# Optimization experiments

Measured on AMD Instinct MI355X. Metric: run time of the kernel, lower is better.

## Reference

```python
import math
import jax, jax.numpy as jnp
import numpy as np

# --- model constants (from TECAN.__init__ defaults) ---
N = 180
DT = 0.02
SIGMA = 40.0
V_PREF = 22.0
RHO_DEG = 0.5
K = 0.0005
WR = 0.94
W_VS = 0.2
TAU = 1.0
RHO_W = 1.0 / RHO_DEG  # 2.0

B, T = 256, 1024


def _circ(a, b):
    return (a - b + 180.0) % 360.0 - 180.0


def setup_inputs() -> dict:
    key = jax.random.key(0)
    k_vel, k_bv, k_ro = jax.random.split(key, 3)

    xs = jnp.linspace(-180.0, 180.0 - 1.0 / RHO_DEG, N)
    coeff = WR / (math.sqrt(2 * math.pi) * SIGMA) * RHO_W
    gauss = lambda d: jnp.exp(-d ** 2 / (2 * SIGMA ** 2))
    W_r = coeff * gauss(_circ(xs[:, None], xs[None, :]))
    W_plus = coeff * gauss(_circ(xs[:, None], xs[None, :] + V_PREF))
    W_minus = coeff * gauss(_circ(xs[:, None], xs[None, :] - V_PREF))

    U_peak = WR * (1 + math.sqrt(1 - 0.896 ** 2 / WR ** 2)) / (4 * math.sqrt(math.pi) * K * SIGMA)
    u_s0 = U_peak * jnp.exp(-xs ** 2 / (4 * SIGMA ** 2))
    h_init = jnp.concatenate([u_s0, jnp.zeros_like(u_s0), jnp.zeros_like(u_s0)])  # [3N]

    vel = jax.random.normal(k_vel, (B, T, 1), dtype=jnp.float32)
    B_v = jax.random.normal(k_bv, (1,), dtype=jnp.float32) / 10.0
    # torch Linear(N,1,bias=False) init: U(-1/sqrt(N), 1/sqrt(N))
    readout_W = jax.random.uniform(k_ro, (1, N), dtype=jnp.float32,
                                   minval=-1.0 / math.sqrt(N), maxval=1.0 / math.sqrt(N))
    return {"vel": vel, "B_v": B_v, "readout_W": readout_W,
            "W_r": W_r, "W_plus": W_plus, "W_minus": W_minus, "h_init": h_init}


def _rates_s(u_s):
    up = jnp.maximum(u_s, 0.0)
    num = up ** 2
    return num / (1.0 + K * RHO_W * jnp.sum(num, axis=-1, keepdims=True))


def reference(vel, B_v, readout_W, W_r, W_plus, W_minus, h_init):
    n = W_r.shape[0]

    def step(h, v_t):
        # h: [B, 3N], v_t: [B, 1]
        u_s, u_p, u_m = h[:, :n], h[:, n:2 * n], h[:, 2 * n:]
        v = v_t * B_v  # [B,1]
        r_s = _rates_s(u_s)
        r_p = jnp.maximum((10.0 + v) * u_p, 0.0)
        r_m = jnp.maximum((10.0 - v) * u_m, 0.0)
        rec = r_s @ W_r.T + r_p @ W_plus.T + r_m @ W_minus.T
        du_s = (-u_s + RHO_W * rec) / TAU
        du_p = (-u_p + W_VS * r_s) / TAU
        du_m = (-u_m + W_VS * r_s) / TAU
        h_new = h + DT * jnp.concatenate([du_s, du_p, du_m], axis=-1)
        out_t = _rates_s(h_new[:, :n]) @ readout_W.T  # [B,1]
        return h_new, out_t

    h0 = jnp.broadcast_to(h_init[None, :], (vel.shape[0], h_init.shape[0]))
    vel_t = jnp.swapaxes(vel, 0, 1)  # [T,B,1]
    _, outs = jax.lax.scan(step, h0, vel_t)  # outs: [T,B,1]
    return jnp.swapaxes(outs, 0, 1)  # [B,T,1]
```

## Files before the change

kernel.cpp:

```cpp
#include <hip/hip_runtime.h>
#include <math.h>

#define NN 180
#define TSTEPS 1024

typedef float v2f __attribute__((ext_vector_type(2)));
__device__ __forceinline__ v2f bc(float s) { v2f r; r.x = s; r.y = s; return r; }
__device__ __forceinline__ v2f mk2(float a, float b) { v2f r; r.x = a; r.y = b; return r; }
__device__ __forceinline__ v2f pkfma(v2f a, v2f b, v2f c) { return __builtin_elementwise_fma(a, b, c); }

template<int CTRL>
__device__ __forceinline__ float dpp_add_b(float x) {
    int y = __builtin_amdgcn_update_dpp(0, __builtin_bit_cast(int, x),
                                        CTRL, 0xF, 0xF, true);
    return x + __builtin_bit_cast(float, y);
}
__device__ __forceinline__ float rl63(float x) {
    return __builtin_bit_cast(float,
        __builtin_amdgcn_readlane(__builtin_bit_cast(int, x), 63));
}
__device__ __forceinline__ float wsum64(float x) {
    x = dpp_add_b<0xB1>(x); x = dpp_add_b<0x4E>(x); x = dpp_add_b<0x141>(x);
    x = dpp_add_b<0x140>(x); x = dpp_add_b<0x142>(x); x = dpp_add_b<0x143>(x);
    return rl63(x);
}

__global__ __launch_bounds__(64, 1) void ring_sim(
    const float* __restrict__ vel,
    const float* __restrict__ B_v,
    const float* __restrict__ ro_w,
    const float* __restrict__ W_r,
    const float* __restrict__ h_init,
    float* __restrict__ out)
{
    const int b = blockIdx.x;
    const int l = threadIdx.x;

    __shared__ float lds_v8[TSTEPS + 2];
    __shared__ v2f   zh[4 * TSTEPS + 5 * 64 + 8];

    {
        const float s = B_v[0] * 0.008f;
        for (int i = l; i < TSTEPS; i += 64)
            lds_v8[i] = vel[b * TSTEPS + i] * s;
        if (l < 2) lds_v8[TSTEPS + l] = 0.f;
    }

    float us0[3], w0[3], ro3[3], kk[3];
    int   dj[3];
    #pragma unroll
    for (int c = 0; c < 3; ++c) {
        int d = l + 64 * c;
        bool okc = (d < NN);
        dj[c]  = okc ? d : 0;
        us0[c] = okc ? h_init[d]              : 0.f;
        w0[c]  = okc ? h_init[NN + d] * 250.f : 0.f;
        ro3[c] = okc ? ro_w[d]                : 0.f;
        kk[c]  = okc ? W_r[d * NN]            : 0.f;
    }

    float Ra[7], Rb[7];
    float a_[4], bb[4], Wa[4], Wb[4], g[4];
    #pragma unroll
    for (int n = 0; n < 7; ++n) {
        float sc = 0.f, ss = 0.f, sk = 0.f, uc = 0.f, usn = 0.f, wc = 0.f, wsn = 0.f;
        #pragma unroll
        for (int c = 0; c < 3; ++c) {
            float ang = 0.0349065850398865915f * (float)((n * dj[c]) % NN);
            float cn = cosf(ang), sn = sinf(ang);
            sc = fmaf(ro3[c], cn, sc);  ss = fmaf(ro3[c], sn, ss);
            if (n < 4) {
                sk  = fmaf(kk[c],  cn, sk);
                uc  = fmaf(us0[c], cn, uc);  usn = fmaf(us0[c], sn, usn);
                wc  = fmaf(w0[c],  cn, wc);  wsn = fmaf(w0[c],  sn, wsn);
            }
        }
        Ra[n] = ((n == 0) ? 1.f : 2.f) * wsum64(sc);
        Rb[n] = 2.f * wsum64(ss);
        if (n < 4) {
            g[n]  = 0.04f * wsum64(sk);
            a_[n] = wsum64(uc)  * (1.f / 180.f);
            bb[n] = wsum64(usn) * (1.f / 180.f);
            Wa[n] = wsum64(wc)  * (1.f / 180.f);
            Wb[n] = wsum64(wsn) * (1.f / 180.f);
        }
    }

    const float w11 = 0.38397243543875251f;
    const float C110 = 0.08f;
    const float C111 = 0.08f * cosf(w11),       s111 = sinf(w11);
    const float C112 = 0.08f * cosf(2.f * w11), s112 = sinf(2.f * w11);
    const float C113 = 0.08f * cosf(3.f * w11), s113 = sinf(3.f * w11);

    float a0 = a_[0];
    v2f z1 = mk2(a_[1], bb[1]), z2 = mk2(a_[2], bb[2]), z3 = mk2(a_[3], bb[3]);
    const float g0 = g[0];
    const float gi1 = 2.f * g[1], gi2 = 2.f * g[2], gi3 = 2.f * g[3];
    float Wt0 = g0 * Wa[0];
    v2f Wt1 = mk2(g[1] * Wa[1], g[1] * Wb[1]);
    v2f Wt2 = mk2(g[2] * Wa[2], g[2] * Wb[2]);
    v2f Wt3 = mk2(g[3] * Wa[3], g[3] * Wb[3]);

    v2f* zp = (l == 0) ? &zh[0] : &zh[4 * TSTEPS + 5 * l];
    const int zstep = (l == 0) ? 4 : 0;
    const float* vp = &lds_v8[1];

    __builtin_amdgcn_wave_barrier();

    float v_use = lds_v8[0];

    #pragma unroll 2
    for (int t = 0; t < TSTEPS; ++t) {
        const float A1 = z1.x, B1 = z1.y, A2 = z2.x, B2 = z2.y, A3 = z3.x, B3 = z3.y;

        v2f s = z1 * z1; s = pkfma(z2, z2, s); s = pkfma(z3, z3, s);
        const float d0 = fmaf(a0, a0, 2.f * (s.x + s.y));

        float d1r = a0 * A1; d1r = fmaf(A1, A2, d1r); d1r = fmaf(B1, B2, d1r);
        d1r = fmaf(A2, A3, d1r); d1r = fmaf(B2, B3, d1r);
        float d1i = a0 * B1; d1i = fmaf(A1, B2, d1i); d1i = fmaf(-B1, A2, d1i);
        d1i = fmaf(A2, B3, d1i); d1i = fmaf(-B2, A3, d1i);

        float P = A1 * A1; P = fmaf(-B1, B1, P);
        float d2r = a0 * A2; d2r = fmaf(A1, A3, d2r); d2r = fmaf(B1, B3, d2r);
        d2r = fmaf(0.5f, P, d2r);
        float d2i = a0 * B2; d2i = fmaf(A1, B3, d2i); d2i = fmaf(-B1, A3, d2i);
        d2i = fmaf(A1, B1, d2i);

        float d3r = a0 * A3; d3r = fmaf(A1, A2, d3r); d3r = fmaf(-B1, B2, d3r);
        float d3i = a0 * B3; d3i = fmaf(A1, B2, d3i); d3i = fmaf(B1, A2, d3i);

        const float inv = __builtin_amdgcn_rcpf(fmaf(d0, 0.18f, 1.0f));

        const float v = v_use;
        v_use = *vp; ++vp;
        const float t1 = v * s111, t2 = v * s112, t3 = v * s113;

        const float q0i = g0 * inv, q1i = gi1 * inv, q2i = gi2 * inv, q3i = gi3 * inv;
        const float gr0  = q0i * d0;
        const v2f   gr1  = mk2(q1i * d1r, q1i * d1i);
        const v2f   gr2  = mk2(q2i * d2r, q2i * d2i);
        const v2f   gr3  = mk2(q3i * d3r, q3i * d3i);

        float u0 = fmaf(C110, Wt0, gr0);
        float u1x = fmaf(C111, Wt1.x, gr1.x); u1x = fmaf(-t1, Wt1.y, u1x);
        float u1y = fmaf(C111, Wt1.y, gr1.y); u1y = fmaf( t1, Wt1.x, u1y);
        float u2x = fmaf(C112, Wt2.x, gr2.x); u2x = fmaf(-t2, Wt2.y, u2x);
        float u2y = fmaf(C112, Wt2.y, gr2.y); u2y = fmaf( t2, Wt2.x, u2y);
        float u3x = fmaf(C113, Wt3.x, gr3.x); u3x = fmaf(-t3, Wt3.y, u3x);
        float u3y = fmaf(C113, Wt3.y, gr3.y); u3y = fmaf( t3, Wt3.x, u3y);

        Wt0 = fmaf(0.98f, Wt0, gr0);
        Wt1 = pkfma(bc(0.98f), Wt1, gr1);
        Wt2 = pkfma(bc(0.98f), Wt2, gr2);
        Wt3 = pkfma(bc(0.98f), Wt3, gr3);

        a0 = fmaf(0.98f, a0, u0);
        z1 = pkfma(bc(0.98f), z1, mk2(u1x, u1y));
        z2 = pkfma(bc(0.98f), z2, mk2(u2x, u2y));
        z3 = pkfma(bc(0.98f), z3, mk2(u3x, u3y));

        zp[0] = z1;
        zp[1] = z2;
        zp[2] = z3;
        zp[3] = mk2(a0, a0);
        zp += zstep;
    }

    __builtin_amdgcn_wave_barrier();

    #pragma unroll
    for (int k = 0; k < TSTEPS / 64; ++k) {
        const int t = 64 * k + l;
        v2f Z1 = zh[4 * t + 0], Z2 = zh[4 * t + 1], Z3 = zh[4 * t + 2];
        const float A0 = zh[4 * t + 3].x;
        const float A1 = Z1.x, B1 = Z1.y, A2 = Z2.x, B2 = Z2.y, A3 = Z3.x, B3 = Z3.y;

        float n2 = A1 * A1; n2 = fmaf(B1, B1, n2); n2 = fmaf(A2, A2, n2);
        n2 = fmaf(B2, B2, n2); n2 = fmaf(A3, A3, n2); n2 = fmaf(B3, B3, n2);
        float D0 = fmaf(A0, A0, 2.f * n2);
        float p1 = A0 * A1; p1 = fmaf(A1, A2, p1); p1 = fmaf(B1, B2, p1);
        p1 = fmaf(A2, A3, p1); p1 = fmaf(B2, B3, p1);
        float D1 = 2.f * p1;
        float p2 = A0 * A2; p2 = fmaf(A1, A3, p2); p2 = fmaf(B1, B3, p2);
        float D2 = fmaf(A1, A1, fmaf(-B1, B1, 2.f * p2));
        float p3 = A1 * A2; p3 = fmaf(-B1, B2, p3); p3 = fmaf(A0, A3, p3);
        float D3 = 2.f * p3;
        float p4 = A1 * A3; p4 = fmaf(-B1, B3, p4);
        float D4 = fmaf(A2, A2, fmaf(-B2, B2, 2.f * p4));
        float p5 = A2 * A3; p5 = fmaf(-B2, B3, p5);
        float D5 = 2.f * p5;
        float D6 = fmaf(A3, A3, -(B3 * B3));
        float q1 = A0 * B1; q1 = fmaf(A1, B2, q1); q1 = fmaf(-A2, B1, q1);
        q1 = fmaf(A2, B3, q1); q1 = fmaf(-A3, B2, q1);
        float e1 = 2.f * q1;
        float q2_ = A1 * B1; q2_ = fmaf(A0, B2, q2_); q2_ = fmaf(A1, B3, q2_);
        q2_ = fmaf(-A3, B1, q2_);
        float e2 = 2.f * q2_;
        float q3 = A1 * B2; q3 = fmaf(A2, B1, q3); q3 = fmaf(A0, B3, q3);
        float e3 = 2.f * q3;
        float q4 = A2 * B2; q4 = fmaf(A1, B3, q4); q4 = fmaf(A3, B1, q4);
        float e4 = 2.f * q4;
        float q5 = A2 * B3; q5 = fmaf(A3, B2, q5);
        float e5 = 2.f * q5;
        float e6 = 2.f * (A3 * B3);

        const float inv = __builtin_amdgcn_rcpf(fmaf(D0, 0.18f, 1.0f));
        float dq = D0 * Ra[0];
        dq = fmaf(D1, Ra[1], dq); dq = fmaf(e1, Rb[1], dq);
        dq = fmaf(D2, Ra[2], dq); dq = fmaf(e2, Rb[2], dq);
        dq = fmaf(D3, Ra[3], dq); dq = fmaf(e3, Rb[3], dq);
        dq = fmaf(D4, Ra[4], dq); dq = fmaf(e4, Rb[4], dq);
        dq = fmaf(D5, Ra[5], dq); dq = fmaf(e5, Rb[5], dq);
        dq = fmaf(D6, Ra[6], dq); dq = fmaf(e6, Rb[6], dq);

        out[b * TSTEPS + t] = dq * inv;
    }
}

extern "C" void kernel_launch(void* const* d_in, const int* in_sizes, int n_in,
                              void* d_out, int out_size, void* d_ws, size_t ws_size,
                              hipStream_t stream) {
    const float* vel    = (const float*)d_in[0];
    const float* B_v    = (const float*)d_in[1];
    const float* ro_w   = (const float*)d_in[2];
    const float* W_r    = (const float*)d_in[3];
    const float* h_init = (const float*)d_in[6];

    const int B = in_sizes[0] / TSTEPS;
    ring_sim<<<dim3(B), dim3(64), 0, stream>>>(vel, B_v, ro_w, W_r, h_init, (float*)d_out);
}
```

Measured before the change: 154.0 us.

## Map one batch sequence per lane instead of one wavefront per sequence

Before, each block handled one sequence: a single lane ran the recurrence serially while 63 lanes idled, then the readout was computed in parallel from an LDS history. Now each lane runs a full sequence independently, with B/64 blocks. The readout is fused into the time loop, velocities are read and outputs written as float4. This removes the LDS history and idle lanes, but launches only B/64 blocks (4 for B=256), so very few CUs are used. Each lane's serial chain also grows because the readout math is now inside the loop.

```diff
diff --git a/kernel.cpp b/kernel.cpp
--- a/kernel.cpp
+++ b/kernel.cpp
@@ -25,7 +25,7 @@
     return rl63(x);
 }
 
-__global__ __launch_bounds__(64, 1) void ring_sim(
+__global__ __launch_bounds__(64, 1) void ring_lane(
     const float* __restrict__ vel,
     const float* __restrict__ B_v,
     const float* __restrict__ ro_w,
@@ -35,16 +35,7 @@
 {
     const int b = blockIdx.x;
     const int l = threadIdx.x;
-
-    __shared__ float lds_v8[TSTEPS + 2];
-    __shared__ v2f   zh[4 * TSTEPS + 5 * 64 + 8];
-
-    {
-        const float s = B_v[0] * 0.008f;
-        for (int i = l; i < TSTEPS; i += 64)
-            lds_v8[i] = vel[b * TSTEPS + i] * s;
-        if (l < 2) lds_v8[TSTEPS + l] = 0.f;
-    }
+    const int seq = b * 64 + l;
 
     float us0[3], w0[3], ro3[3], kk[3];
     int   dj[3];
@@ -86,11 +77,21 @@
         }
     }
 
+    const float Ra0 = Ra[0];
+    const float Ra21 = 2.f * Ra[1], Rb21 = 2.f * Rb[1];
+    const float Ra22 = 2.f * Ra[2], Rb22 = 2.f * Rb[2];
+    const float Ra23 = 2.f * Ra[3], Rb23 = 2.f * Rb[3];
+    const float Ra24 = 2.f * Ra[4], Rb24 = 2.f * Rb[4];
+    const float Ra25 = 2.f * Ra[5], Rb25 = 2.f * Rb[5];
+    const float Ra6  = Ra[6],       Rb26 = 2.f * Rb[6];
+    const float RaP1 = Ra[2], RaP2 = Ra[4];
+
     const float w11 = 0.38397243543875251f;
+    const float vs   = B_v[0] * 0.008f;
     const float C110 = 0.08f;
-    const float C111 = 0.08f * cosf(w11),       s111 = sinf(w11);
-    const float C112 = 0.08f * cosf(2.f * w11), s112 = sinf(2.f * w11);
-    const float C113 = 0.08f * cosf(3.f * w11), s113 = sinf(3.f * w11);
+    const float C111 = 0.08f * cosf(w11),       svs1 = vs * sinf(w11);
+    const float C112 = 0.08f * cosf(2.f * w11), svs2 = vs * sinf(2.f * w11);
+    const float C113 = 0.08f * cosf(3.f * w11), svs3 = vs * sinf(3.f * w11);
 
     float a0 = a_[0];
     v2f z1 = mk2(a_[1], bb[1]), z2 = mk2(a_[2], bb[2]), z3 = mk2(a_[3], bb[3]);
@@ -101,120 +102,111 @@
     v2f Wt2 = mk2(g[2] * Wa[2], g[2] * Wb[2]);
     v2f Wt3 = mk2(g[3] * Wa[3], g[3] * Wb[3]);
 
-    v2f* zp = (l == 0) ? &zh[0] : &zh[4 * TSTEPS + 5 * l];
-    const int zstep = (l == 0) ? 4 : 0;
-    const float* vp = &lds_v8[1];
-
-    __builtin_amdgcn_wave_barrier();
-
-    float v_use = lds_v8[0];
-
-    #pragma unroll 2
-    for (int t = 0; t < TSTEPS; ++t) {
-        const float A1 = z1.x, B1 = z1.y, A2 = z2.x, B2 = z2.y, A3 = z3.x, B3 = z3.y;
-
-        v2f s = z1 * z1; s = pkfma(z2, z2, s); s = pkfma(z3, z3, s);
-        const float d0 = fmaf(a0, a0, 2.f * (s.x + s.y));
-
-        float d1r = a0 * A1; d1r = fmaf(A1, A2, d1r); d1r = fmaf(B1, B2, d1r);
-        d1r = fmaf(A2, A3, d1r); d1r = fmaf(B2, B3, d1r);
-        float d1i = a0 * B1; d1i = fmaf(A1, B2, d1i); d1i = fmaf(-B1, A2, d1i);
-        d1i = fmaf(A2, B3, d1i); d1i = fmaf(-B2, A3, d1i);
-
-        float P = A1 * A1; P = fmaf(-B1, B1, P);
-        float d2r = a0 * A2; d2r = fmaf(A1, A3, d2r); d2r = fmaf(B1, B3, d2r);
-        d2r = fmaf(0.5f, P, d2r);
-        float d2i = a0 * B2; d2i = fmaf(A1, B3, d2i); d2i = fmaf(-B1, A3, d2i);
-        d2i = fmaf(A1, B1, d2i);
-
-        float d3r = a0 * A3; d3r = fmaf(A1, A2, d3r); d3r = fmaf(-B1, B2, d3r);
-        float d3i = a0 * B3; d3i = fmaf(A1, B2, d3i); d3i = fmaf(B1, A2, d3i);
-
-        const float inv = __builtin_amdgcn_rcpf(fmaf(d0, 0.18f, 1.0f));
-
-        const float v = v_use;
-        v_use = *vp; ++vp;
-        const float t1 = v * s111, t2 = v * s112, t3 = v * s113;
-
-        const float q0i = g0 * inv, q1i = gi1 * inv, q2i = gi2 * inv, q3i = gi3 * inv;
-        const float gr0  = q0i * d0;
-        const v2f   gr1  = mk2(q1i * d1r, q1i * d1i);
-        const v2f   gr2  = mk2(q2i * d2r, q2i * d2i);
-        const v2f   gr3  = mk2(q3i * d3r, q3i * d3i);
-
-        float u0 = fmaf(C110, Wt0, gr0);
-        float u1x = fmaf(C111, Wt1.x, gr1.x); u1x = fmaf(-t1, Wt1.y, u1x);
-        float u1y = fmaf(C111, Wt1.y, gr1.y); u1y = fmaf( t1, Wt1.x, u1y);
-        float u2x = fmaf(C112, Wt2.x, gr2.x); u2x = fmaf(-t2, Wt2.y, u2x);
-        float u2y = fmaf(C112, Wt2.y, gr2.y); u2y = fmaf( t2, Wt2.x, u2y);
-        float u3x = fmaf(C113, Wt3.x, gr3.x); u3x = fmaf(-t3, Wt3.y, u3x);
-        float u3y = fmaf(C113, Wt3.y, gr3.y); u3y = fmaf( t3, Wt3.x, u3y);
+    const float4* vptr = (const float4*)(vel + seq * TSTEPS);
+    float4*       optr = (float4*)(out + seq * TSTEPS);
+
+    auto update = [&](float v, float inv,
+                      float d0, float d1r, float d1i, float d2r, float d2i,
+                      float d3r, float d3i) {
+        const float t1 = v * svs1, t2 = v * svs2, t3 = v * svs3;
+        const float gv0 = g0 * inv, gv1 = gi1 * inv, gv2 = gi2 * inv, gv3 = gi3 * inv;
+        const float gr0 = gv0 * d0;
+        const float g1x = gv1 * d1r, g1y = gv1 * d1i;
+        const float g2x = gv2 * d2r, g2y = gv2 * d2i;
+        const float g3x = gv3 * d3r, g3y = gv3 * d3i;
+
+        float u0  = fmaf(C110, Wt0, gr0);
+        float u1x = fmaf(C111, Wt1.x, g1x); u1x = fmaf(-t1, Wt1.y, u1x);
+        float u1y = fmaf(C111, Wt1.y, g1y); u1y = fmaf( t1, Wt1.x, u1y);
+        float u2x = fmaf(C112, Wt2.x, g2x); u2x = fmaf(-t2, Wt2.y, u2x);
+        float u2y = fmaf(C112, Wt2.y, g2y); u2y = fmaf( t2, Wt2.x, u2y);
+        float u3x = fmaf(C113, Wt3.x, g3x); u3x = fmaf(-t3, Wt3.y, u3x);
+        float u3y = fmaf(C113, Wt3.y, g3y); u3y = fmaf( t3, Wt3.x, u3y);
 
         Wt0 = fmaf(0.98f, Wt0, gr0);
-        Wt1 = pkfma(bc(0.98f), Wt1, gr1);
-        Wt2 = pkfma(bc(0.98f), Wt2, gr2);
-        Wt3 = pkfma(bc(0.98f), Wt3, gr3);
+        Wt1 = pkfma(bc(0.98f), Wt1, mk2(g1x, g1y));
+        Wt2 = pkfma(bc(0.98f), Wt2, mk2(g2x, g2y));
+        Wt3 = pkfma(bc(0.98f), Wt3, mk2(g3x, g3y));
 
         a0 = fmaf(0.98f, a0, u0);
         z1 = pkfma(bc(0.98f), z1, mk2(u1x, u1y));
         z2 = pkfma(bc(0.98f), z2, mk2(u2x, u2y));
         z3 = pkfma(bc(0.98f), z3, mk2(u3x, u3y));
-
-        zp[0] = z1;
-        zp[1] = z2;
-        zp[2] = z3;
-        zp[3] = mk2(a0, a0);
-        zp += zstep;
-    }
-
-    __builtin_amdgcn_wave_barrier();
-
-    #pragma unroll
-    for (int k = 0; k < TSTEPS / 64; ++k) {
-        const int t = 64 * k + l;
-        v2f Z1 = zh[4 * t + 0], Z2 = zh[4 * t + 1], Z3 = zh[4 * t + 2];
-        const float A0 = zh[4 * t + 3].x;
-        const float A1 = Z1.x, B1 = Z1.y, A2 = Z2.x, B2 = Z2.y, A3 = Z3.x, B3 = Z3.y;
-
-        float n2 = A1 * A1; n2 = fmaf(B1, B1, n2); n2 = fmaf(A2, A2, n2);
-        n2 = fmaf(B2, B2, n2); n2 = fmaf(A3, A3, n2); n2 = fmaf(B3, B3, n2);
-        float D0 = fmaf(A0, A0, 2.f * n2);
-        float p1 = A0 * A1; p1 = fmaf(A1, A2, p1); p1 = fmaf(B1, B2, p1);
+    };
+
+    float4 vcur = vptr[0];
+
+    {
+        const float A1 = z1.x, B1 = z1.y, A2 = z2.x, B2 = z2.y, A3 = z3.x, B3 = z3.y;
+        v2f s = z1 * z1; s = pkfma(z2, z2, s); s = pkfma(z3, z3, s);
+        float sh = s.x + s.y;
+        float d0 = fmaf(a0, a0, sh + sh);
+        float p1 = a0 * A1; p1 = fmaf(A1, A2, p1); p1 = fmaf(B1, B2, p1);
         p1 = fmaf(A2, A3, p1); p1 = fmaf(B2, B3, p1);
-        float D1 = 2.f * p1;
-        float p2 = A0 * A2; p2 = fmaf(A1, A3, p2); p2 = fmaf(B1, B3, p2);
-        float D2 = fmaf(A1, A1, fmaf(-B1, B1, 2.f * p2));
-        float p3 = A1 * A2; p3 = fmaf(-B1, B2, p3); p3 = fmaf(A0, A3, p3);
-        float D3 = 2.f * p3;
-        float p4 = A1 * A3; p4 = fmaf(-B1, B3, p4);
-        float D4 = fmaf(A2, A2, fmaf(-B2, B2, 2.f * p4));
-        float p5 = A2 * A3; p5 = fmaf(-B2, B3, p5);
-        float D5 = 2.f * p5;
-        float D6 = fmaf(A3, A3, -(B3 * B3));
-        float q1 = A0 * B1; q1 = fmaf(A1, B2, q1); q1 = fmaf(-A2, B1, q1);
+        float q1 = a0 * B1; q1 = fmaf(A1, B2, q1); q1 = fmaf(-A2, B1, q1);
         q1 = fmaf(A2, B3, q1); q1 = fmaf(-A3, B2, q1);
-        float e1 = 2.f * q1;
-        float q2_ = A1 * B1; q2_ = fmaf(A0, B2, q2_); q2_ = fmaf(A1, B3, q2_);
-        q2_ = fmaf(-A3, B1, q2_);
-        float e2 = 2.f * q2_;
-        float q3 = A1 * B2; q3 = fmaf(A2, B1, q3); q3 = fmaf(A0, B3, q3);
-        float e3 = 2.f * q3;
-        float q4 = A2 * B2; q4 = fmaf(A1, B3, q4); q4 = fmaf(A3, B1, q4);
-        float e4 = 2.f * q4;
-        float q5 = A2 * B3; q5 = fmaf(A3, B2, q5);
-        float e5 = 2.f * q5;
-        float e6 = 2.f * (A3 * B3);
-
-        const float inv = __builtin_amdgcn_rcpf(fmaf(D0, 0.18f, 1.0f));
-        float dq = D0 * Ra[0];
-        dq = fmaf(D1, Ra[1], dq); dq = fmaf(e1, Rb[1], dq);
-        dq = fmaf(D2, Ra[2], dq); dq = fmaf(e2, Rb[2], dq);
-        dq = fmaf(D3, Ra[3], dq); dq = fmaf(e3, Rb[3], dq);
-        dq = fmaf(D4, Ra[4], dq); dq = fmaf(e4, Rb[4], dq);
-        dq = fmaf(D5, Ra[5], dq); dq = fmaf(e5, Rb[5], dq);
-        dq = fmaf(D6, Ra[6], dq); dq = fmaf(e6, Rb[6], dq);
-
-        out[b * TSTEPS + t] = dq * inv;
+        float P1 = A1 * A1; P1 = fmaf(-B1, B1, P1);
+        float p2 = a0 * A2; p2 = fmaf(A1, A3, p2); p2 = fmaf(B1, B3, p2);
+        float d2r = fmaf(0.5f, P1, p2);
+        float q2 = A1 * B1; q2 = fmaf(a0, B2, q2); q2 = fmaf(A1, B3, q2);
+        q2 = fmaf(-A3, B1, q2);
+        float p3 = A1 * A2; p3 = fmaf(-B1, B2, p3); p3 = fmaf(a0, A3, p3);
+        float q3 = A1 * B2; q3 = fmaf(A2, B1, q3); q3 = fmaf(a0, B3, q3);
+        const float inv = __builtin_amdgcn_rcpf(fmaf(d0, 0.18f, 1.0f));
+        update(vcur.x, inv, d0, p1, q1, d2r, q2, p3, q3);
+    }
+
+    #pragma unroll 1
+    for (int blk = 0; blk < TSTEPS / 4; ++blk) {
+        const float4 vnext = (blk < TSTEPS / 4 - 1) ? vptr[blk + 1] : vcur;
+        float4 o;
+        #pragma unroll
+        for (int c = 0; c < 4; ++c) {
+            const float A1 = z1.x, B1 = z1.y, A2 = z2.x, B2 = z2.y, A3 = z3.x, B3 = z3.y;
+
+            v2f s = z1 * z1; s = pkfma(z2, z2, s); s = pkfma(z3, z3, s);
+            float sh = s.x + s.y;
+            float d0 = fmaf(a0, a0, sh + sh);
+            float p1 = a0 * A1; p1 = fmaf(A1, A2, p1); p1 = fmaf(B1, B2, p1);
+            p1 = fmaf(A2, A3, p1); p1 = fmaf(B2, B3, p1);
+            float q1 = a0 * B1; q1 = fmaf(A1, B2, q1); q1 = fmaf(-A2, B1, q1);
+            q1 = fmaf(A2, B3, q1); q1 = fmaf(-A3, B2, q1);
+            float P1 = A1 * A1; P1 = fmaf(-B1, B1, P1);
+            float p2 = a0 * A2; p2 = fmaf(A1, A3, p2); p2 = fmaf(B1, B3, p2);
+            float q2 = A1 * B1; q2 = fmaf(a0, B2, q2); q2 = fmaf(A1, B3, q2);
+            q2 = fmaf(-A3, B1, q2);
+            float p3 = A1 * A2; p3 = fmaf(-B1, B2, p3); p3 = fmaf(a0, A3, p3);
+            float q3 = A1 * B2; q3 = fmaf(A2, B1, q3); q3 = fmaf(a0, B3, q3);
+            float p4 = A1 * A3; p4 = fmaf(-B1, B3, p4);
+            float q4 = A2 * B2; q4 = fmaf(A1, B3, q4); q4 = fmaf(A3, B1, q4);
+            float P2 = A2 * A2; P2 = fmaf(-B2, B2, P2);
+            float p5 = A2 * A3; p5 = fmaf(-B2, B3, p5);
+            float q5 = A2 * B3; q5 = fmaf(A3, B2, q5);
+            float P3 = A3 * A3; P3 = fmaf(-B3, B3, P3);
+            float w6 = A3 * B3;
+
+            const float inv = __builtin_amdgcn_rcpf(fmaf(d0, 0.18f, 1.0f));
+
+            float dq = d0 * Ra0;
+            dq = fmaf(p1, Ra21, dq); dq = fmaf(q1, Rb21, dq);
+            dq = fmaf(P1, RaP1, dq); dq = fmaf(p2, Ra22, dq); dq = fmaf(q2, Rb22, dq);
+            dq = fmaf(p3, Ra23, dq); dq = fmaf(q3, Rb23, dq);
+            dq = fmaf(P2, RaP2, dq); dq = fmaf(p4, Ra24, dq); dq = fmaf(q4, Rb24, dq);
+            dq = fmaf(p5, Ra25, dq); dq = fmaf(q5, Rb25, dq);
+            dq = fmaf(P3, Ra6, dq);  dq = fmaf(w6, Rb26, dq);
+
+            if (c == 0) o.x = dq * inv;
+            if (c == 1) o.y = dq * inv;
+            if (c == 2) o.z = dq * inv;
+            if (c == 3) o.w = dq * inv;
+
+            const float vv = (c == 0) ? vcur.y : (c == 1) ? vcur.z
+                           : (c == 2) ? vcur.w : vnext.x;
+            const float d2r = fmaf(0.5f, P1, p2);
+            update(vv, inv, d0, p1, q1, d2r, q2, p3, q3);
+        }
+        optr[blk] = o;
+        vcur = vnext;
     }
 }
 
@@ -228,5 +220,5 @@
     const float* h_init = (const float*)d_in[6];
 
     const int B = in_sizes[0] / TSTEPS;
-    ring_sim<<<dim3(B), dim3(64), 0, stream>>>(vel, B_v, ro_w, W_r, h_init, (float*)d_out);
-}
+    ring_lane<<<dim3(B / 64), dim3(64), 0, stream>>>(vel, B_v, ro_w, W_r, h_init, (float*)d_out);
+}
```

Result: slower. 205.1 us (+33.1%).

## Pack complex recurrence into inline-asm packed FMAs and stream velocities from global

Applied to the files above, without the earlier changes.

The serial per-timestep recurrence now does its complex products with hand-written v_pk_fma_f32 inline assembly using op_sel/neg modifiers, so each real/imag pair takes one packed op instead of two scalar FMAs. The velocity staging pass into LDS is dropped: velocities are read as float4 directly from global memory one block ahead, with B_v scaling folded into the sine constants. The state history layout changes to 8 floats per step. The aim is a shorter dependent critical path per step, at the cost of correctness depending on hand-written operand-select encodings and exposure to global load latency inside the loop.

```diff
diff --git a/kernel.cpp b/kernel.cpp
--- a/kernel.cpp
+++ b/kernel.cpp
@@ -8,6 +8,19 @@
 __device__ __forceinline__ v2f bc(float s) { v2f r; r.x = s; r.y = s; return r; }
 __device__ __forceinline__ v2f mk2(float a, float b) { v2f r; r.x = a; r.y = b; return r; }
 __device__ __forceinline__ v2f pkfma(v2f a, v2f b, v2f c) { return __builtin_elementwise_fma(a, b, c); }
+
+#define CFMA_A(acc, z, w) \
+    asm("v_pk_fma_f32 %0, %1, %2, %0 op_sel:[0,0,0] op_sel_hi:[0,1,1]" \
+        : "+v"(acc) : "v"(z), "v"(w))
+#define CFMA_B(acc, z, w) \
+    asm("v_pk_fma_f32 %0, %1, %2, %0 op_sel:[1,1,0] op_sel_hi:[1,0,1] neg_lo:[1,0,0]" \
+        : "+v"(acc) : "v"(z), "v"(w))
+#define CFMA_BC(acc, z, w) \
+    asm("v_pk_fma_f32 %0, %1, %2, %0 op_sel:[1,1,0] op_sel_hi:[1,0,1] neg_hi:[1,0,0]" \
+        : "+v"(acc) : "v"(z), "v"(w))
+#define JFMA(acc, t, w) \
+    asm("v_pk_fma_f32 %0, %1, %2, %0 op_sel:[0,1,0] op_sel_hi:[0,0,1] neg_lo:[0,1,0]" \
+        : "+v"(acc) : "v"(t), "v"(w))
 
 template<int CTRL>
 __device__ __forceinline__ float dpp_add_b(float x) {
@@ -36,15 +49,8 @@
     const int b = blockIdx.x;
     const int l = threadIdx.x;
 
-    __shared__ float lds_v8[TSTEPS + 2];
-    __shared__ v2f   zh[4 * TSTEPS + 5 * 64 + 8];
-
-    {
-        const float s = B_v[0] * 0.008f;
-        for (int i = l; i < TSTEPS; i += 64)
-            lds_v8[i] = vel[b * TSTEPS + i] * s;
-        if (l < 2) lds_v8[TSTEPS + l] = 0.f;
-    }
+    __shared__ float hist[8 * TSTEPS];
+    __shared__ float dump[34 * 64 + 8];
 
     float us0[3], w0[3], ro3[3], kk[3];
     int   dj[3];
@@ -59,8 +65,7 @@
         kk[c]  = okc ? W_r[d * NN]            : 0.f;
     }
 
-    float Ra[7], Rb[7];
-    float a_[4], bb[4], Wa[4], Wb[4], g[4];
+    float Ra[7], Rb[7], a_[4], bb[4], Wa[4], Wb[4], g[4];
     #pragma unroll
     for (int n = 0; n < 7; ++n) {
         float sc = 0.f, ss = 0.f, sk = 0.f, uc = 0.f, usn = 0.f, wc = 0.f, wsn = 0.f;
@@ -87,93 +92,103 @@
     }
 
     const float w11 = 0.38397243543875251f;
+    const float vs   = B_v[0] * 0.008f;
     const float C110 = 0.08f;
-    const float C111 = 0.08f * cosf(w11),       s111 = sinf(w11);
-    const float C112 = 0.08f * cosf(2.f * w11), s112 = sinf(2.f * w11);
-    const float C113 = 0.08f * cosf(3.f * w11), s113 = sinf(3.f * w11);
+    const v2f C1d = bc(0.08f * cosf(w11)),       svs1d = bc(vs * sinf(w11));
+    const v2f C2d = bc(0.08f * cosf(2.f * w11)), svs2d = bc(vs * sinf(2.f * w11));
+    const v2f C3d = bc(0.08f * cosf(3.f * w11)), svs3d = bc(vs * sinf(3.f * w11));
+    const float g0 = g[0];
+    const v2f gi1d = bc(2.f * g[1]), gi2d = bc(2.f * g[2]), gi3d = bc(2.f * g[3]);
+    const v2f p98d = bc(0.98f), halfd = bc(0.5f);
 
     float a0 = a_[0];
+    v2f a0d = bc(a0);
     v2f z1 = mk2(a_[1], bb[1]), z2 = mk2(a_[2], bb[2]), z3 = mk2(a_[3], bb[3]);
-    const float g0 = g[0];
-    const float gi1 = 2.f * g[1], gi2 = 2.f * g[2], gi3 = 2.f * g[3];
     float Wt0 = g0 * Wa[0];
     v2f Wt1 = mk2(g[1] * Wa[1], g[1] * Wb[1]);
     v2f Wt2 = mk2(g[2] * Wa[2], g[2] * Wb[2]);
     v2f Wt3 = mk2(g[3] * Wa[3], g[3] * Wb[3]);
 
-    v2f* zp = (l == 0) ? &zh[0] : &zh[4 * TSTEPS + 5 * l];
-    const int zstep = (l == 0) ? 4 : 0;
-    const float* vp = &lds_v8[1];
+    float* hp = (l == 0) ? hist : (dump + 34 * l);
+    const int hstep = (l == 0) ? 8 : 0;
+
+    const float4* vptr = (const float4*)(vel + (size_t)b * TSTEPS);
+
+    auto step = [&](float vv) {
+        v2f s = z1 * z1; s = pkfma(z2, z2, s); s = pkfma(z3, z3, s);
+        const float sh = s.x + s.y;
+        const float d0 = fmaf(a0, a0, sh + sh);
+
+        v2f d1 = a0d * z1;
+        CFMA_A(d1, z1, z2); CFMA_BC(d1, z1, z2);
+        CFMA_A(d1, z2, z3); CFMA_BC(d1, z2, z3);
+
+        v2f d2 = a0d * z2;
+        CFMA_A(d2, z1, z3); CFMA_BC(d2, z1, z3);
+        v2f zh1 = halfd * z1;
+        CFMA_A(d2, zh1, z1); CFMA_B(d2, zh1, z1);
+
+        v2f d3 = a0d * z3;
+        CFMA_A(d3, z1, z2); CFMA_B(d3, z1, z2);
+
+        const float inv = __builtin_amdgcn_rcpf(fmaf(d0, 0.18f, 1.0f));
+        const v2f invd = bc(inv);
+        const v2f vd   = bc(vv);
+        const v2f td1 = svs1d * vd, td2 = svs2d * vd, td3 = svs3d * vd;
+
+        const float gr0 = (g0 * inv) * d0;
+        const float u0  = fmaf(C110, Wt0, gr0);
+        Wt0 = fmaf(0.98f, Wt0, gr0);
+        a0  = fmaf(0.98f, a0, u0);
+        a0d = bc(a0);
+
+        v2f gv, gr, u;
+        gv = gi1d * invd; gr = gv * d1;
+        u = pkfma(C1d, Wt1, gr); JFMA(u, td1, Wt1);
+        Wt1 = pkfma(p98d, Wt1, gr);
+        z1  = pkfma(p98d, z1, u);
+
+        gv = gi2d * invd; gr = gv * d2;
+        u = pkfma(C2d, Wt2, gr); JFMA(u, td2, Wt2);
+        Wt2 = pkfma(p98d, Wt2, gr);
+        z2  = pkfma(p98d, z2, u);
+
+        gv = gi3d * invd; gr = gv * d3;
+        u = pkfma(C3d, Wt3, gr); JFMA(u, td3, Wt3);
+        Wt3 = pkfma(p98d, Wt3, gr);
+        z3  = pkfma(p98d, z3, u);
+    };
+
+    float4 vcur = vptr[0];
+    step(vcur.x);
+
+    #pragma unroll 1
+    for (int blk = 0; blk < TSTEPS / 4; ++blk) {
+        const float4 vnext = (blk < TSTEPS / 4 - 1) ? vptr[blk + 1] : vcur;
+        #pragma unroll
+        for (int c = 0; c < 4; ++c) {
+            hp[0] = a0;
+            *(v2f*)(hp + 2) = z1;
+            *(v2f*)(hp + 4) = z2;
+            *(v2f*)(hp + 6) = z3;
+            hp += hstep;
+            const float vv = (c == 0) ? vcur.y : (c == 1) ? vcur.z
+                           : (c == 2) ? vcur.w : vnext.x;
+            step(vv);
+        }
+        vcur = vnext;
+    }
 
     __builtin_amdgcn_wave_barrier();
 
-    float v_use = lds_v8[0];
-
-    #pragma unroll 2
-    for (int t = 0; t < TSTEPS; ++t) {
-        const float A1 = z1.x, B1 = z1.y, A2 = z2.x, B2 = z2.y, A3 = z3.x, B3 = z3.y;
-
-        v2f s = z1 * z1; s = pkfma(z2, z2, s); s = pkfma(z3, z3, s);
-        const float d0 = fmaf(a0, a0, 2.f * (s.x + s.y));
-
-        float d1r = a0 * A1; d1r = fmaf(A1, A2, d1r); d1r = fmaf(B1, B2, d1r);
-        d1r = fmaf(A2, A3, d1r); d1r = fmaf(B2, B3, d1r);
-        float d1i = a0 * B1; d1i = fmaf(A1, B2, d1i); d1i = fmaf(-B1, A2, d1i);
-        d1i = fmaf(A2, B3, d1i); d1i = fmaf(-B2, A3, d1i);
-
-        float P = A1 * A1; P = fmaf(-B1, B1, P);
-        float d2r = a0 * A2; d2r = fmaf(A1, A3, d2r); d2r = fmaf(B1, B3, d2r);
-        d2r = fmaf(0.5f, P, d2r);
-        float d2i = a0 * B2; d2i = fmaf(A1, B3, d2i); d2i = fmaf(-B1, A3, d2i);
-        d2i = fmaf(A1, B1, d2i);
-
-        float d3r = a0 * A3; d3r = fmaf(A1, A2, d3r); d3r = fmaf(-B1, B2, d3r);
-        float d3i = a0 * B3; d3i = fmaf(A1, B2, d3i); d3i = fmaf(B1, A2, d3i);
-
-        const float inv = __builtin_amdgcn_rcpf(fmaf(d0, 0.18f, 1.0f));
-
-        const float v = v_use;
-        v_use = *vp; ++vp;
-        const float t1 = v * s111, t2 = v * s112, t3 = v * s113;
-
-        const float q0i = g0 * inv, q1i = gi1 * inv, q2i = gi2 * inv, q3i = gi3 * inv;
-        const float gr0  = q0i * d0;
-        const v2f   gr1  = mk2(q1i * d1r, q1i * d1i);
-        const v2f   gr2  = mk2(q2i * d2r, q2i * d2i);
-        const v2f   gr3  = mk2(q3i * d3r, q3i * d3i);
-
-        float u0 = fmaf(C110, Wt0, gr0);
-        float u1x = fmaf(C111, Wt1.x, gr1.x); u1x = fmaf(-t1, Wt1.y, u1x);
-        float u1y = fmaf(C111, Wt1.y, gr1.y); u1y = fmaf( t1, Wt1.x, u1y);
-        float u2x = fmaf(C112, Wt2.x, gr2.x); u2x = fmaf(-t2, Wt2.y, u2x);
-        float u2y = fmaf(C112, Wt2.y, gr2.y); u2y = fmaf( t2, Wt2.x, u2y);
-        float u3x = fmaf(C113, Wt3.x, gr3.x); u3x = fmaf(-t3, Wt3.y, u3x);
-        float u3y = fmaf(C113, Wt3.y, gr3.y); u3y = fmaf( t3, Wt3.x, u3y);
-
-        Wt0 = fmaf(0.98f, Wt0, gr0);
-        Wt1 = pkfma(bc(0.98f), Wt1, gr1);
-        Wt2 = pkfma(bc(0.98f), Wt2, gr2);
-        Wt3 = pkfma(bc(0.98f), Wt3, gr3);
-
-        a0 = fmaf(0.98f, a0, u0);
-        z1 = pkfma(bc(0.98f), z1, mk2(u1x, u1y));
-        z2 = pkfma(bc(0.98f), z2, mk2(u2x, u2y));
-        z3 = pkfma(bc(0.98f), z3, mk2(u3x, u3y));
-
-        zp[0] = z1;
-        zp[1] = z2;
-        zp[2] = z3;
-        zp[3] = mk2(a0, a0);
-        zp += zstep;
-    }
-
-    __builtin_amdgcn_wave_barrier();
-
-    #pragma unroll
-    for (int k = 0; k < TSTEPS / 64; ++k) {
-        const int t = 64 * k + l;
-        v2f Z1 = zh[4 * t + 0], Z2 = zh[4 * t + 1], Z3 = zh[4 * t + 2];
-        const float A0 = zh[4 * t + 3].x;
+    #pragma unroll 1
+    for (int it = 0; it < TSTEPS / 64; ++it) {
+        const int t = it * 64 + l;
+        const float* hb = hist + 8 * t;
+        const float A0 = hb[0];
+        const v2f Z1 = *(const v2f*)(hb + 2);
+        const v2f Z2 = *(const v2f*)(hb + 4);
+        const v2f Z3 = *(const v2f*)(hb + 6);
         const float A1 = Z1.x, B1 = Z1.y, A2 = Z2.x, B2 = Z2.y, A3 = Z3.x, B3 = Z3.y;
 
         float n2 = A1 * A1; n2 = fmaf(B1, B1, n2); n2 = fmaf(A2, A2, n2);
@@ -214,7 +229,7 @@
         dq = fmaf(D5, Ra[5], dq); dq = fmaf(e5, Rb[5], dq);
         dq = fmaf(D6, Ra[6], dq); dq = fmaf(e6, Rb[6], dq);
 
-        out[b * TSTEPS + t] = dq * inv;
+        out[(size_t)b * TSTEPS + t] = dq * inv;
     }
 }
 
@@ -228,5 +243,6 @@
     const float* h_init = (const float*)d_in[6];
 
     const int B = in_sizes[0] / TSTEPS;
-    ring_sim<<<dim3(B), dim3(64), 0, stream>>>(vel, B_v, ro_w, W_r, h_init, (float*)d_out);
-}
+    ring_sim<<<dim3(B), dim3(64), 0, stream>>>(
+        vel, B_v, ro_w, W_r, h_init, (float*)d_out);
+}
```

New measurement: 143.6 us. -6.7%, faster.
